# Performance work log

Hardware: AMD Instinct MI355X
Metric: run time of the kernel (lower is better)

The kernel has to match this reference:

```python
import jax, jax.numpy as jnp
import numpy as np
from jax import lax

HID = 64
GROUPS = 4
EPS = 1e-5


def group_norm(x, w, b):
    # x: [B, C, H, W], GROUPS groups
    B, C, H, W = x.shape
    xg = x.reshape(B, GROUPS, C // GROUPS, H, W)
    mu = xg.mean(axis=(2, 3, 4), keepdims=True)
    var = xg.var(axis=(2, 3, 4), keepdims=True)
    xn = ((xg - mu) * lax.rsqrt(var + EPS)).reshape(B, C, H, W)
    return xn * w[:, None, None] + b[:, None, None]


def cell_step(x_t, h, c, W, gw, gb):
    # x_t: [B, Cin, H, W]; h, c: [B, HID, H, W]; W: [4*HID, Cin+HID, k, k]
    inp = jnp.concatenate([x_t, h], axis=1)
    gates = lax.conv_general_dilated(inp, W, (1, 1), 'SAME',
                                     dimension_numbers=('NCHW', 'OIHW', 'NCHW'))
    gates = group_norm(gates, gw, gb)
    i, f, o, g = jnp.split(gates, 4, axis=1)
    i, f, o = jax.nn.sigmoid(i), jax.nn.sigmoid(f), jax.nn.sigmoid(o)
    g = jnp.tanh(g)
    c_next = f * c + i * g
    h_next = o * jnp.tanh(c_next)
    return h_next, c_next


def run_direction(xt, W, gw, gb, reverse):
    # xt: [T, B, C, H, W]
    T, B, C, H, Wd = xt.shape
    h0 = jnp.zeros((B, HID, H, Wd), xt.dtype)
    c0 = jnp.zeros_like(h0)

    def step(carry, x_t):
        h, c = carry
        h, c = cell_step(x_t, h, c, W, gw, gb)
        return (h, c), h

    _, hs = lax.scan(step, (h0, c0), xt, reverse=reverse)
    return hs  # [T, B, HID, H, W] in time order


def setup_inputs() -> dict:
    key = jax.random.key(0)
    ks = jax.random.split(key, 12)
    B, T, C, H, W = 4, 16, 64, 64, 64
    k = 3
    G4 = 4 * HID
    x = jax.random.normal(ks[0], (B, T, C, H, W), jnp.float32)
    Wf = jax.random.normal(ks[1], (G4, C + HID, k, k), jnp.float32) * 0.02
    gnf_w = 1.0 + 0.1 * jax.random.normal(ks[2], (G4,), jnp.float32)
    gnf_b = 0.1 * jax.random.normal(ks[3], (G4,), jnp.float32)
    Wb = jax.random.normal(ks[4], (G4, C + HID, k, k), jnp.float32) * 0.02
    gnb_w = 1.0 + 0.1 * jax.random.normal(ks[5], (G4,), jnp.float32)
    gnb_b = 0.1 * jax.random.normal(ks[6], (G4,), jnp.float32)
    Wfu = jax.random.normal(ks[7], (HID, 2 * HID, 1, 1), jnp.float32) * 0.05
    bn_w = 1.0 + 0.1 * jax.random.normal(ks[8], (HID,), jnp.float32)
    bn_b = 0.1 * jax.random.normal(ks[9], (HID,), jnp.float32)
    return {"x": x, "Wf": Wf, "gnf_w": gnf_w, "gnf_b": gnf_b,
            "Wb": Wb, "gnb_w": gnb_w, "gnb_b": gnb_b,
            "Wfu": Wfu, "bn_w": bn_w, "bn_b": bn_b}


def reference(x, Wf, gnf_w, gnf_b, Wb, gnb_w, gnb_b, Wfu, bn_w, bn_b):
    B, T, C, H, W = x.shape
    xt = jnp.transpose(x, (1, 0, 2, 3, 4))  # [T, B, C, H, W]
    hf = run_direction(xt, Wf, gnf_w, gnf_b, reverse=False)
    hb = run_direction(xt, Wb, gnb_w, gnb_b, reverse=True)
    combined = jnp.concatenate([hf, hb], axis=2)  # [T, B, 2*HID, H, W]
    comb = combined.reshape(T * B, 2 * HID, H, W)
    fused = lax.conv_general_dilated(comb, Wfu, (1, 1), 'SAME',
                                     dimension_numbers=('NCHW', 'OIHW', 'NCHW'))
    # BatchNorm2d (training-mode batch statistics), then ReLU
    mu = fused.mean(axis=(0, 2, 3), keepdims=True)
    var = fused.var(axis=(0, 2, 3), keepdims=True)
    fused = (fused - mu) * lax.rsqrt(var + EPS)
    fused = fused * bn_w[:, None, None] + bn_b[:, None, None]
    fused = jax.nn.relu(fused)
    out = fused.reshape(T, B, HID, H, W).transpose(1, 0, 2, 3, 4)
    return out
```

## Files before the change

### kernel.cpp

```cpp
#include <hip/hip_runtime.h>
#include <math.h>

#define PX 4096
#define EPS 1e-5f

typedef __attribute__((ext_vector_type(8))) __bf16 bf16x8;
typedef __attribute__((ext_vector_type(4))) float f32x4;

static __device__ __forceinline__ unsigned short f2b(float f) {
    unsigned int u = __float_as_uint(f);
    u += 0x7FFFu + ((u >> 16) & 1u);
    return (unsigned short)(u >> 16);
}
static __device__ __forceinline__ float b2f(unsigned short u) {
    return __uint_as_float((unsigned int)u << 16);
}
static __device__ __forceinline__ float rcpf(float x) {
    return __builtin_amdgcn_rcpf(x);
}


__global__ __launch_bounds__(256) void pack_kernel(
    const float* __restrict__ Wf, const float* __restrict__ Wb,
    const float* __restrict__ Wfu,
    unsigned short* __restrict__ W2s, unsigned short* __restrict__ wfrag)
{
    int idx = blockIdx.x * 256 + threadIdx.x;
    if (idx < 589824) {
        int within = idx & 2047;
        int grp = idx >> 11;
        int oc = within >> 5;
        int slot = (within >> 3) & 3;
        int j = within & 7;
        int tap = grp % 9;
        int rest = grp / 9;
        int icblk = rest & 3;
        int ocblk = (rest >> 2) & 3;
        int dir = rest >> 4;
        int c = slot ^ ((oc >> 1) & 3);
        int ic = icblk * 32 + c * 8 + j;
        int OC = ocblk * 64 + oc;
        const float* __restrict__ W = dir ? Wb : Wf;
        W2s[idx] = f2b(W[((size_t)OC * 128 + ic) * 9 + tap]);
    } else if (idx < 589824 + 8192) {
        int k = idx - 589824;
        int j = k & 7;
        int l = (k >> 3) & 63;
        int icblk = (k >> 9) & 3;
        int ocb = k >> 11;
        int oc = ocb * 16 + (l & 15);
        int ic = icblk * 32 + (l >> 4) * 8 + j;
        wfrag[k] = f2b(Wfu[oc * 128 + ic]);
    }
}

__global__ __launch_bounds__(256) void xconv_kernel(
    const float* __restrict__ x, unsigned short* __restrict__ xb)
{
    int bt = blockIdx.x >> 6;
    int px0 = (blockIdx.x & 63) * 64;
    __shared__ unsigned short sh[64 * 72];
    int tid = threadIdx.x;
    {
        int px_l = tid & 63;
        int ic4 = tid >> 6;
        const float* __restrict__ src = x + (size_t)bt * 64 * PX + px0 + px_l;
#pragma unroll
        for (int k = 0; k < 16; ++k) {
            int ic = ic4 * 16 + k;
            sh[px_l * 72 + ic] = f2b(src[(size_t)ic * PX]);
        }
    }
    __syncthreads();
    {
        int px_w = tid >> 2;
        int ch = tid & 3;
        uint4 v0 = *reinterpret_cast<const uint4*>(&sh[px_w * 72 + ch * 16]);
        uint4 v1 = *reinterpret_cast<const uint4*>(&sh[px_w * 72 + ch * 16 + 8]);
        unsigned short* dst = xb + ((size_t)bt * PX + px0 + px_w) * 64 + ch * 16;
        *reinterpret_cast<uint4*>(dst) = v0;
        *reinterpret_cast<uint4*>(dst + 8) = v1;
    }
}

__global__ __launch_bounds__(256, 2) void conv_mfma_kernel(
    const unsigned short* __restrict__ xb, const unsigned short* __restrict__ comb_t,
    const unsigned short* __restrict__ W2s,
    unsigned short* __restrict__ gatesb, float* __restrict__ gnstats, int s)
{
    const int dirb = blockIdx.x & 7;
    const int rest = blockIdx.x >> 3;
    const int dir = dirb >> 2, b = dirb & 3;
    const int ocblk = rest >> 4;
    const int pxt = rest & 15;
    const int py0 = (pxt >> 1) * 8;
    const int pxc0 = (pxt & 1) * 32;
    const int t = dir ? (15 - s) : s;
    const int prev_t = dir ? (t + 1) : (t - 1);

    __shared__ __align__(16) unsigned short Wl[9 * 64 * 32];
    __shared__ __align__(16) unsigned short in_s[2][340 * 32];
    __shared__ float red[8];

    const int tid = threadIdx.x;
    const int w = tid >> 6;
    const int l = tid & 63;
    const int l15 = l & 15;
    const int l4 = l >> 4;
    const int wb = tid & ~63;

    const unsigned short* __restrict__ xpx = xb + (size_t)(b * 16 + t) * PX * 64;
    const unsigned short* __restrict__ hpx = comb_t
        + (size_t)(prev_t * 4 + b) * PX * 128 + dir * 64;

    int sg_px[6];
#pragma unroll
    for (int it = 0; it < 6; ++it) {
        int idx = tid + it * 256;
        int pl = idx >> 2;
        int row = (pl * 241) >> 13;
        int col = pl - row * 34;
        int gy = py0 - 1 + row;
        int gx = pxc0 - 1 + col;
        bool valid = (idx < 1360) && ((unsigned)gy < 64u) && ((unsigned)gx < 64u);
        sg_px[it] = valid ? (gy * 64 + gx) : -1;
    }

    f32x4 acc[4][4];
#pragma unroll
    for (int i = 0; i < 4; ++i)
#pragma unroll
        for (int j = 0; j < 4; ++j)
            acc[i][j] = (f32x4){0.f, 0.f, 0.f, 0.f};

    uint4 sreg[6];
    auto stage_load = [&](int icblk) {
        const bool useh = icblk >= 2;
        const unsigned short* __restrict__ srcpx = useh
            ? (hpx + (icblk - 2) * 32) : (xpx + icblk * 32);
        const int rec = useh ? 128 : 64;
        const bool zero = useh && (s == 0);
        const int c = tid & 3;
#pragma unroll
        for (int it = 0; it < 6; ++it) {
            uint4 v = make_uint4(0u, 0u, 0u, 0u);
            if (sg_px[it] >= 0 && !zero)
                v = *reinterpret_cast<const uint4*>(
                    srcpx + (size_t)sg_px[it] * rec + c * 8);
            sreg[it] = v;
        }
    };
    auto stage_write = [&](int buf) {
#pragma unroll
        for (int it = 0; it < 6; ++it) {
            int idx = tid + it * 256;
            if (idx < 1360) {
                int c = idx & 3;
                int pl = idx >> 2;
                int woff = pl * 32 + ((c ^ ((pl >> 1) & 3)) * 8);
                *reinterpret_cast<uint4*>(&in_s[buf][woff]) = sreg[it];
            }
        }
    };
    auto issueW = [&](int icblk) {
        const unsigned short* __restrict__ wsrc = W2s
            + ((size_t)((dir * 4 + ocblk) * 4 + icblk) * 9) * 2048;
#pragma unroll
        for (int it = 0; it < 9; ++it) {
            __builtin_amdgcn_global_load_lds(
                (const __attribute__((address_space(1))) void*)
                    (wsrc + (size_t)(tid + it * 256) * 8),
                (__attribute__((address_space(3))) void*)
                    (&Wl[(wb + it * 256) * 8]),
                16, 0, 0);
        }
    };

    stage_load(0);
    stage_write(0);

    for (int icblk = 0; icblk < 4; ++icblk) {
        __syncthreads();
        issueW(icblk);
        __syncthreads();
        if (icblk < 3) stage_load(icblk + 1);
        const unsigned short* __restrict__ ib = in_s[icblk & 1];

#pragma unroll
        for (int tap = 0; tap < 9; ++tap) {
            const int dy = tap / 3, dx = tap % 3;
            bf16x8 av[4], bv[4];
#pragma unroll
            for (int mi = 0; mi < 4; ++mi) {
                int oc = mi * 16 + l15;
                int aoff = tap * 2048 + oc * 32 + ((l4 ^ ((oc >> 1) & 3)) * 8);
                av[mi] = *reinterpret_cast<const bf16x8*>(&Wl[aoff]);
            }
#pragma unroll
            for (int ni = 0; ni < 4; ++ni) {
                int nr = ni >> 1, nc = ni & 1;
                int pl = (2 * w + nr + dy) * 34 + nc * 16 + l15 + dx;
                int boff = pl * 32 + ((l4 ^ ((pl >> 1) & 3)) * 8);
                bv[ni] = *reinterpret_cast<const bf16x8*>(&ib[boff]);
            }
#pragma unroll
            for (int mi = 0; mi < 4; ++mi)
#pragma unroll
                for (int ni = 0; ni < 4; ++ni)
                    acc[mi][ni] = __builtin_amdgcn_mfma_f32_16x16x32_bf16(
                        av[mi], bv[ni], acc[mi][ni], 0, 0, 0);
        }

        if (icblk < 3) stage_write((icblk + 1) & 1);
    }

    float s1 = 0.f, s2 = 0.f;
    unsigned short* __restrict__ gbase = gatesb
        + ((size_t)dirb * 256 + (size_t)ocblk * 64) * PX;
#pragma unroll
    for (int mi = 0; mi < 4; ++mi)
#pragma unroll
        for (int ni = 0; ni < 4; ++ni) {
            int nr = ni >> 1, nc = ni & 1;
            int px = (py0 + 2 * w + nr) * 64 + pxc0 + nc * 16 + l15;
#pragma unroll
            for (int j = 0; j < 4; ++j) {
                float v = acc[mi][ni][j];
                int oc = mi * 16 + l4 * 4 + j;
                gbase[(size_t)oc * PX + px] = f2b(v);
                s1 += v;
                s2 += v * v;
            }
        }
    for (int off = 32; off; off >>= 1) {
        s1 += __shfl_down(s1, off);
        s2 += __shfl_down(s2, off);
    }
    if (l == 0) { red[w * 2] = s1; red[w * 2 + 1] = s2; }
    __syncthreads();
    if (tid == 0) {
        float a = red[0] + red[2] + red[4] + red[6];
        float q = red[1] + red[3] + red[5] + red[7];
        float* slot = gnstats + (((size_t)(s * 2 + dir) * 4 + b) * 4 + ocblk) * 2;
        atomicAdd(slot, a);
        atomicAdd(slot + 1, q);
    }
}

__global__ __launch_bounds__(256) void point_kernel2(
    const unsigned short* __restrict__ gatesb, const float* __restrict__ gnstats,
    const float* __restrict__ gnf_w, const float* __restrict__ gnf_b,
    const float* __restrict__ gnb_w, const float* __restrict__ gnb_b,
    unsigned short* __restrict__ cbuf, unsigned short* __restrict__ comb_t, int s)
{
    int dirb = blockIdx.x & 7;
    int idx = (blockIdx.x >> 3) * 256 + threadIdx.x;
    int pxl = idx & 7;
    int o8 = (idx >> 3) & 7;
    int pxh = idx >> 6;
    int px = pxh * 8 + pxl;
    int dir = dirb >> 2, b = dirb & 3;

    __shared__ float gwl[256], gbl[256], mrs[8];
    int tid = threadIdx.x;
    {
        const float* __restrict__ gw = dir ? gnb_w : gnf_w;
        const float* __restrict__ gb = dir ? gnb_b : gnf_b;
        gwl[tid] = gw[tid];
        gbl[tid] = gb[tid];
    }
    if (tid < 4) {
        const float* slot = gnstats + ((size_t)(s * 2 + dir) * 4 + b) * 8 + tid * 2;
        const float invN = 1.0f / 262144.0f;
        float mean = slot[0] * invN;
        float var = slot[1] * invN - mean * mean;
        mrs[tid * 2] = mean;
        mrs[tid * 2 + 1] = rsqrtf(var + EPS);
    }
    __syncthreads();

    const unsigned short* __restrict__ gbase = gatesb + (size_t)dirb * 256 * PX + px;
    size_t cbase = ((size_t)dirb * 64 + o8 * 8) * PX + px;
    float m0 = mrs[0], r0 = mrs[1], m1 = mrs[2], r1 = mrs[3];
    float m2 = mrs[4], r2 = mrs[5], m3 = mrs[6], r3 = mrs[7];

    unsigned int packed[4];
#pragma unroll
    for (int cc = 0; cc < 8; ++cc) {
        int ch = o8 * 8 + cc;
        float g0 = b2f(gbase[(size_t)(ch) * PX]);
        float g1 = b2f(gbase[(size_t)(64 + ch) * PX]);
        float g2 = b2f(gbase[(size_t)(128 + ch) * PX]);
        float g3 = b2f(gbase[(size_t)(192 + ch) * PX]);
        float v0 = (g0 - m0) * r0 * gwl[ch] + gbl[ch];
        float v1 = (g1 - m1) * r1 * gwl[64 + ch] + gbl[64 + ch];
        float v2 = (g2 - m2) * r2 * gwl[128 + ch] + gbl[128 + ch];
        float v3 = (g3 - m3) * r3 * gwl[192 + ch] + gbl[192 + ch];
        float ig = rcpf(1.f + __expf(-v0));
        float fg = rcpf(1.f + __expf(-v1));
        float og = rcpf(1.f + __expf(-v2));
        float gg = 1.f - 2.f * rcpf(1.f + __expf(2.f * v3));
        float cold = b2f(cbuf[cbase + (size_t)cc * PX]);
        float cnew = fg * cold + ig * gg;
        float th = 1.f - 2.f * rcpf(1.f + __expf(2.f * cnew));
        float hnew = og * th;
        cbuf[cbase + (size_t)cc * PX] = f2b(cnew);
        unsigned int hb = (unsigned int)f2b(hnew);
        if (cc & 1) packed[cc >> 1] |= hb << 16;
        else        packed[cc >> 1] = hb;
    }
    int t = dir ? (15 - s) : s;
    size_t co = ((size_t)(t * 4 + b) * PX + px) * 128 + dir * 64 + o8 * 8;
    *reinterpret_cast<uint4*>(comb_t + co) =
        make_uint4(packed[0], packed[1], packed[2], packed[3]);
}

__global__ __launch_bounds__(256) void fuse_stats2_kernel(
    const unsigned short* __restrict__ comb_t,
    const unsigned short* __restrict__ wfrag, float* __restrict__ bnparts)
{
    int n = blockIdx.x >> 4, pxb = blockIdx.x & 15;
    int tid = threadIdx.x;
    int w = tid >> 6, l = tid & 63;
    int l15 = l & 15, l4 = l >> 4;

    bf16x8 B[4][4];
#pragma unroll
    for (int ocb = 0; ocb < 4; ++ocb)
#pragma unroll
        for (int icblk = 0; icblk < 4; ++icblk)
            B[ocb][icblk] = *reinterpret_cast<const bf16x8*>(
                wfrag + (((ocb * 4 + icblk) * 64 + l) * 8));

    f32x4 acc[4][4];
#pragma unroll
    for (int i = 0; i < 4; ++i)
#pragma unroll
        for (int j = 0; j < 4; ++j)
            acc[i][j] = (f32x4){0.f, 0.f, 0.f, 0.f};

    int px0 = pxb * 256 + w * 64;
    const unsigned short* __restrict__ cb = comb_t + (size_t)n * PX * 128;
#pragma unroll
    for (int ps = 0; ps < 4; ++ps) {
        const unsigned short* ab = cb + (size_t)(px0 + ps * 16 + l15) * 128 + l4 * 8;
        bf16x8 A[4];
#pragma unroll
        for (int icblk = 0; icblk < 4; ++icblk)
            A[icblk] = *reinterpret_cast<const bf16x8*>(ab + icblk * 32);
#pragma unroll
        for (int icblk = 0; icblk < 4; ++icblk)
#pragma unroll
            for (int ocb = 0; ocb < 4; ++ocb)
                acc[ps][ocb] = __builtin_amdgcn_mfma_f32_16x16x32_bf16(
                    A[icblk], B[ocb][icblk], acc[ps][ocb], 0, 0, 0);
    }

    float s1[4] = {0, 0, 0, 0}, s2[4] = {0, 0, 0, 0};
#pragma unroll
    for (int ps = 0; ps < 4; ++ps)
#pragma unroll
        for (int ocb = 0; ocb < 4; ++ocb)
#pragma unroll
            for (int j = 0; j < 4; ++j) {
                float v = acc[ps][ocb][j];
                s1[ocb] += v;
                s2[ocb] += v * v;
            }
#pragma unroll
    for (int ocb = 0; ocb < 4; ++ocb) {
        s1[ocb] += __shfl_down(s1[ocb], 32);
        s1[ocb] += __shfl_down(s1[ocb], 16);
        s2[ocb] += __shfl_down(s2[ocb], 32);
        s2[ocb] += __shfl_down(s2[ocb], 16);
    }
    __shared__ float sred[4][4][16][2];
    if (l < 16)
#pragma unroll
        for (int ocb = 0; ocb < 4; ++ocb) {
            sred[w][ocb][l][0] = s1[ocb];
            sred[w][ocb][l][1] = s2[ocb];
        }
    __syncthreads();
    if (tid < 128) {
        int oc = tid >> 1, isq = tid & 1;
        float v = sred[0][oc >> 4][oc & 15][isq] + sred[1][oc >> 4][oc & 15][isq]
                + sred[2][oc >> 4][oc & 15][isq] + sred[3][oc >> 4][oc & 15][isq];
        atomicAdd(bnparts + (blockIdx.x & 7) * 128 + tid, v);
    }
}

__global__ __launch_bounds__(256) void bn_apply2_kernel(
    const unsigned short* __restrict__ comb_t,
    const unsigned short* __restrict__ wfrag, const float* __restrict__ bnparts,
    const float* __restrict__ bn_w, const float* __restrict__ bn_b,
    float* __restrict__ out)
{
    int n = blockIdx.x >> 4, pxb = blockIdx.x & 15;
    int tid = threadIdx.x;
    int w = tid >> 6, l = tid & 63;
    int l15 = l & 15, l4 = l >> 4;

    __shared__ float sc[64], sh[64];
    if (tid < 64) {
        const float invN = 1.0f / 262144.0f;
        float S = 0.f, Q = 0.f;
#pragma unroll
        for (int p = 0; p < 8; ++p) {
            S += bnparts[p * 128 + tid * 2];
            Q += bnparts[p * 128 + tid * 2 + 1];
        }
        float mean = S * invN;
        float var = Q * invN - mean * mean;
        float scale = rsqrtf(var + EPS) * bn_w[tid];
        sc[tid] = scale;
        sh[tid] = bn_b[tid] - mean * scale;
    }

    bf16x8 B[4][4];
#pragma unroll
    for (int ocb = 0; ocb < 4; ++ocb)
#pragma unroll
        for (int icblk = 0; icblk < 4; ++icblk)
            B[ocb][icblk] = *reinterpret_cast<const bf16x8*>(
                wfrag + (((ocb * 4 + icblk) * 64 + l) * 8));
    __syncthreads();

    f32x4 acc[4][4];
#pragma unroll
    for (int i = 0; i < 4; ++i)
#pragma unroll
        for (int j = 0; j < 4; ++j)
            acc[i][j] = (f32x4){0.f, 0.f, 0.f, 0.f};

    int px0 = pxb * 256 + w * 64;
    const unsigned short* __restrict__ cb = comb_t + (size_t)n * PX * 128;
#pragma unroll
    for (int ps = 0; ps < 4; ++ps) {
        const unsigned short* ab = cb + (size_t)(px0 + ps * 16 + l15) * 128 + l4 * 8;
        bf16x8 A[4];
#pragma unroll
        for (int icblk = 0; icblk < 4; ++icblk)
            A[icblk] = *reinterpret_cast<const bf16x8*>(ab + icblk * 32);
#pragma unroll
        for (int icblk = 0; icblk < 4; ++icblk)
#pragma unroll
            for (int ocb = 0; ocb < 4; ++ocb)
                acc[ps][ocb] = __builtin_amdgcn_mfma_f32_16x16x32_bf16(
                    A[icblk], B[ocb][icblk], acc[ps][ocb], 0, 0, 0);
    }

    int t = n >> 2, bb = n & 3;
#pragma unroll
    for (int ps = 0; ps < 4; ++ps)
#pragma unroll
        for (int ocb = 0; ocb < 4; ++ocb) {
            int oc = ocb * 16 + l15;
            float scale = sc[oc], shift = sh[oc];
            float4 v;
            v.x = fmaxf(acc[ps][ocb][0] * scale + shift, 0.f);
            v.y = fmaxf(acc[ps][ocb][1] * scale + shift, 0.f);
            v.z = fmaxf(acc[ps][ocb][2] * scale + shift, 0.f);
            v.w = fmaxf(acc[ps][ocb][3] * scale + shift, 0.f);
            float* op = out + ((size_t)((bb * 16 + t) * 64 + oc)) * PX
                      + px0 + ps * 16 + l4 * 4;
            *reinterpret_cast<float4*>(op) = v;
        }
}

extern "C" void kernel_launch(void* const* d_in, const int* in_sizes, int n_in,
                              void* d_out, int out_size, void* d_ws, size_t ws_size,
                              hipStream_t stream) {
    const float* x     = (const float*)d_in[0];
    const float* Wf    = (const float*)d_in[1];
    const float* gnf_w = (const float*)d_in[2];
    const float* gnf_b = (const float*)d_in[3];
    const float* Wb    = (const float*)d_in[4];
    const float* gnb_w = (const float*)d_in[5];
    const float* gnb_b = (const float*)d_in[6];
    const float* Wfu   = (const float*)d_in[7];
    const float* bn_w  = (const float*)d_in[8];
    const float* bn_b  = (const float*)d_in[9];
    float* out = (float*)d_out;

    float* ws = (float*)d_ws;
    unsigned short* comb_t = (unsigned short*)ws;
    unsigned short* gatesb = (unsigned short*)(ws + 16777216);
    unsigned short* cbuf   = (unsigned short*)(ws + 20971520);
    float* gnstats = ws + 22020096;
    float* bnparts = ws + 22021120;
    unsigned short* W2s   = (unsigned short*)(ws + 22022144);
    unsigned short* wfrag = (unsigned short*)(ws + 22317056);
    unsigned short* xb    = (unsigned short*)(ws + 22321152);

    hipMemsetAsync(cbuf, 0, (size_t)(1048576 + 2048) * 4, stream);

    pack_kernel<<<2336, 256, 0, stream>>>(Wf, Wb, Wfu, W2s, wfrag);
    xconv_kernel<<<4096, 256, 0, stream>>>(x, xb);

    for (int s = 0; s < 16; ++s) {
        conv_mfma_kernel<<<512, 256, 0, stream>>>(
            xb, comb_t, W2s, gatesb, gnstats, s);
        point_kernel2<<<1024, 256, 0, stream>>>(
            gatesb, gnstats, gnf_w, gnf_b, gnb_w, gnb_b, cbuf, comb_t, s);
    }
    fuse_stats2_kernel<<<1024, 256, 0, stream>>>(comb_t, wfrag, bnparts);
    bn_apply2_kernel<<<1024, 256, 0, stream>>>(comb_t, wfrag, bnparts, bn_w, bn_b, out);
}
```

Baseline: 560.2 us.

## Prefetch conv weights through registers to overlap with MFMA compute

```diff
diff --git a/kernel.cpp b/kernel.cpp
--- a/kernel.cpp
+++ b/kernel.cpp
@@ -107,11 +107,12 @@
     const int l = tid & 63;
     const int l15 = l & 15;
     const int l4 = l >> 4;
-    const int wb = tid & ~63;
 
     const unsigned short* __restrict__ xpx = xb + (size_t)(b * 16 + t) * PX * 64;
     const unsigned short* __restrict__ hpx = comb_t
         + (size_t)(prev_t * 4 + b) * PX * 128 + dir * 64;
+    const unsigned short* __restrict__ wblk = W2s
+        + (size_t)(dir * 4 + ocblk) * 4 * 9 * 2048 + (size_t)tid * 8;
 
     int sg_px[6];
 #pragma unroll
@@ -134,6 +135,7 @@
             acc[i][j] = (f32x4){0.f, 0.f, 0.f, 0.f};
 
     uint4 sreg[6];
+    uint4 wreg[9];
     auto stage_load = [&](int icblk) {
         const bool useh = icblk >= 2;
         const unsigned short* __restrict__ srcpx = useh
@@ -162,28 +164,29 @@
             }
         }
     };
-    auto issueW = [&](int icblk) {
-        const unsigned short* __restrict__ wsrc = W2s
-            + ((size_t)((dir * 4 + ocblk) * 4 + icblk) * 9) * 2048;
-#pragma unroll
-        for (int it = 0; it < 9; ++it) {
-            __builtin_amdgcn_global_load_lds(
-                (const __attribute__((address_space(1))) void*)
-                    (wsrc + (size_t)(tid + it * 256) * 8),
-                (__attribute__((address_space(3))) void*)
-                    (&Wl[(wb + it * 256) * 8]),
-                16, 0, 0);
-        }
+    auto wload = [&](int icblk) {
+        const unsigned short* __restrict__ wsrc = wblk + (size_t)icblk * 9 * 2048;
+#pragma unroll
+        for (int it = 0; it < 9; ++it)
+            wreg[it] = *reinterpret_cast<const uint4*>(wsrc + it * 2048);
     };
-
+    auto wwrite = [&]() {
+#pragma unroll
+        for (int it = 0; it < 9; ++it)
+            *reinterpret_cast<uint4*>(&Wl[(tid + it * 256) * 8]) = wreg[it];
+    };
+
+    wload(0);
     stage_load(0);
+    wwrite();
     stage_write(0);
+    __syncthreads();
 
     for (int icblk = 0; icblk < 4; ++icblk) {
-        __syncthreads();
-        issueW(icblk);
-        __syncthreads();
-        if (icblk < 3) stage_load(icblk + 1);
+        if (icblk < 3) {
+            wload(icblk + 1);
+            stage_load(icblk + 1);
+        }
         const unsigned short* __restrict__ ib = in_s[icblk & 1];
 
 #pragma unroll
@@ -211,7 +214,12 @@
                         av[mi], bv[ni], acc[mi][ni], 0, 0, 0);
         }
 
-        if (icblk < 3) stage_write((icblk + 1) & 1);
+        __syncthreads();
+        if (icblk < 3) {
+            wwrite();
+            stage_write((icblk + 1) & 1);
+            __syncthreads();
+        }
     }
 
     float s1 = 0.f, s2 = 0.f;
```

After: 782.8 us. +39.7%, slower.
